# Kernel tuning notes

Measured on AMD Instinct MI355X. Metric: run time of the kernel, lower is better.

Reference implementation:

```python
import jax, jax.numpy as jnp
import numpy as np

N, E, D, H = 100000, 600000, 128, 512  # nodes, edges, latent_dim, 4*latent_dim


def setup_inputs() -> dict:
    key = jax.random.key(0)
    ks = jax.random.split(key, 9)
    s = 0.05
    return {
        "z": jax.random.normal(ks[0], (N, D), dtype=jnp.float32),
        "edge_index": jax.random.randint(ks[1], (2, E), 0, N, dtype=jnp.int64),
        "Wg": jax.random.normal(ks[2], (D, D), dtype=jnp.float32) * s,
        "Ws": jax.random.normal(ks[3], (D, D), dtype=jnp.float32) * s,
        "bg": jnp.zeros((D,), dtype=jnp.float32),
        "W1": jax.random.normal(ks[4], (D, H), dtype=jnp.float32) * s,
        "b1": jnp.zeros((H,), dtype=jnp.float32),
        "W2": jax.random.normal(ks[5], (H, H), dtype=jnp.float32) * s,
        "b2": jnp.zeros((H,), dtype=jnp.float32),
        "W3": jax.random.normal(ks[6], (H, D), dtype=jnp.float32) * s,
        "b3": jnp.zeros((D,), dtype=jnp.float32),
    }


def reference(z, edge_index, Wg, Ws, bg, W1, b1, W2, b2, W3, b3):
    src, dst = edge_index[0], edge_index[1]
    n = z.shape[0]
    # GNN: gather neighbor features along edges, mean-aggregate at dst
    msgs = z[src]                                   # (E, D) gather
    agg = jax.ops.segment_sum(msgs, dst, num_segments=n)  # (N, D) scatter-add
    deg = jax.ops.segment_sum(jnp.ones((src.shape[0],), z.dtype), dst, num_segments=n)
    agg = agg / jnp.maximum(deg, 1.0)[:, None]      # mean aggregation
    h = jax.nn.relu(agg @ Wg + z @ Ws + bg)          # (N, D) graph conv output
    # MLP: Linear -> Tanh -> Linear -> Tanh -> Linear
    h = jnp.tanh(h @ W1 + b1)
    h = jnp.tanh(h @ W2 + b2)
    return h @ W3 + b3                               # dz/dt: (N, D)
```

## Files before the change

kernel.cpp:

```cpp
#include <hip/hip_runtime.h>
#include <hip/hip_fp16.h>


typedef _Float16 f16;
typedef __attribute__((ext_vector_type(4))) _Float16 f16x4;
typedef __attribute__((ext_vector_type(8))) _Float16 f16x8;
typedef __attribute__((ext_vector_type(4))) float f32x4;

__device__ __forceinline__ void async_load16(const void* g, void* lds) {
  __builtin_amdgcn_global_load_lds(
      (const __attribute__((address_space(1))) void*)g,
      (__attribute__((address_space(3))) void*)lds, 16, 0, 0);
}

__device__ __forceinline__ float fast_tanh(float x) {
  float a = fabsf(x);
  float e = __expf(-2.0f * a);
  float r = (1.0f - e) * __builtin_amdgcn_rcpf(1.0f + e);
  return copysignf(r, x);
}

__global__ __launch_bounds__(256) void scan_partial(const int* __restrict__ degi,
                                                    int* __restrict__ bsum, int N) {
  __shared__ int lds[256];
  int b = blockIdx.x, t = threadIdx.x;
  int s = 0;
#pragma unroll
  for (int j = 0; j < 4; ++j) {
    int idx = b * 1024 + t * 4 + j;
    if (idx < N) s += degi[idx];
  }
  lds[t] = s;
  __syncthreads();
  for (int off = 128; off > 0; off >>= 1) {
    if (t < off) lds[t] += lds[t + off];
    __syncthreads();
  }
  if (t == 0) bsum[b] = lds[0];
}

__global__ __launch_bounds__(256) void scan_final(
    const int* __restrict__ degi, const int* __restrict__ bsum,
    int* __restrict__ row_start, int* __restrict__ cursor, int nb, int N, int E) {
  __shared__ int lds[256];
  __shared__ int sboff;
  int b = blockIdx.x, t = threadIdx.x;
  lds[t] = (t < b && t < nb) ? bsum[t] : 0;
  __syncthreads();
  for (int off = 128; off > 0; off >>= 1) {
    if (t < off) lds[t] += lds[t + off];
    __syncthreads();
  }
  if (t == 0) {
    sboff = lds[0];
    if (b == 0) row_start[N] = E;
  }
  __syncthreads();

  int base = b * 1024;
  int v[4];
  int s = 0;
#pragma unroll
  for (int j = 0; j < 4; ++j) {
    int idx = base + t * 4 + j;
    v[j] = (idx < N) ? degi[idx] : 0;
    s += v[j];
  }
  lds[t] = s;
  __syncthreads();
  for (int off = 1; off < 256; off <<= 1) {
    int x = lds[t];
    int y = (t >= off) ? lds[t - off] : 0;
    __syncthreads();
    lds[t] = x + y;
    __syncthreads();
  }
  int pre = sboff + lds[t] - s;
#pragma unroll
  for (int j = 0; j < 4; ++j) {
    int idx = base + t * 4 + j;
    if (idx < N) { row_start[idx] = pre; cursor[idx] = pre; pre += v[j]; }
  }
}

__global__ __launch_bounds__(256) void fill_adj(const int* __restrict__ src,
                                                const int* __restrict__ dst,
                                                int* __restrict__ cursor,
                                                int* __restrict__ adj, int E) {
  int e = blockIdx.x * 256 + threadIdx.x;
  if (e >= E) return;
  int p = atomicAdd(&cursor[dst[e]], 1);
  adj[p] = src[e];
}

__global__ __launch_bounds__(256) void fused_prep(
    const int* __restrict__ dst, int* __restrict__ degi, int E,
    const float* __restrict__ Wg, const float* __restrict__ Ws,
    const float* __restrict__ W1, const float* __restrict__ W2,
    const float* __restrict__ W3, f16* __restrict__ wgs, f16* __restrict__ wt1,
    f16* __restrict__ wt2, f16* __restrict__ wt3,
    const float* __restrict__ z, f16* __restrict__ z16, f16* __restrict__ Xc,
    int n4) {
  int i0 = blockIdx.x * 256 + threadIdx.x;
  int stride = gridDim.x * 256;
  for (int i = i0; i < n4; i += stride) {
    float4 v = *(const float4*)(z + 4 * (long long)i);
    f16x4 c;
    c[0] = (f16)v.x; c[1] = (f16)v.y; c[2] = (f16)v.z; c[3] = (f16)v.w;
    *(f16x4*)(z16 + 4 * (long long)i) = c;
    int node = i >> 5, sl = i & 31;
    *(f16x4*)(Xc + (long long)node * 256 + 128 + 4 * sl) = c;
  }
  for (int i = i0; i < E; i += stride) atomicAdd(&degi[dst[i]], 1);
  for (int i = i0; i < 425984; i += stride) {
    if (i < 32768) {
      int n = i >> 8, k = i & 255;
      wgs[i] = (f16)((k < 128) ? Wg[k * 128 + n] : Ws[(k - 128) * 128 + n]);
    } else if (i < 98304) {
      int j = i - 32768, c = j >> 7, k = j & 127;
      wt1[j] = (f16)W1[k * 512 + c];
    } else if (i < 360448) {
      int j = i - 98304, c = j >> 9, k = j & 511;
      wt2[j] = (f16)W2[k * 512 + c];
    } else {
      int j = i - 360448, c = j >> 9, k = j & 511;
      wt3[j] = (f16)W3[k * 128 + c];
    }
  }
}

__global__ __launch_bounds__(256) void gather_xcat(
    const f16* __restrict__ z16, const int* __restrict__ row_start,
    const int* __restrict__ adj, f16* __restrict__ Xc, int N) {
  int node = (blockIdx.x * 256 + threadIdx.x) >> 5;
  if (node >= N) return;
  int lane = threadIdx.x & 31;
  int beg = row_start[node], end = row_start[node + 1];
  float a0 = 0, a1 = 0, a2 = 0, a3 = 0;
#pragma unroll
  for (int j = 0; j < 8; ++j) {
    int idx = beg + j;
    bool vld = idx < end;
    int nb = adj[vld ? idx : beg];
    f16x4 x = *(const f16x4*)(z16 + (long long)nb * 128 + 4 * lane);
    float w = vld ? 1.0f : 0.0f;
    a0 += w * (float)x[0]; a1 += w * (float)x[1];
    a2 += w * (float)x[2]; a3 += w * (float)x[3];
  }
  int i = beg + 8;
  if (i < end) {
    float b0 = 0, b1 = 0, b2 = 0, b3 = 0;
    float c0 = 0, c1 = 0, c2 = 0, c3 = 0;
    float d0 = 0, d1 = 0, d2 = 0, d3 = 0;
    for (; i + 4 <= end; i += 4) {
      int n0 = adj[i], n1 = adj[i + 1], n2 = adj[i + 2], n3 = adj[i + 3];
      f16x4 v0 = *(const f16x4*)(z16 + (long long)n0 * 128 + 4 * lane);
      f16x4 v1 = *(const f16x4*)(z16 + (long long)n1 * 128 + 4 * lane);
      f16x4 v2 = *(const f16x4*)(z16 + (long long)n2 * 128 + 4 * lane);
      f16x4 v3 = *(const f16x4*)(z16 + (long long)n3 * 128 + 4 * lane);
      a0 += (float)v0[0]; a1 += (float)v0[1]; a2 += (float)v0[2]; a3 += (float)v0[3];
      b0 += (float)v1[0]; b1 += (float)v1[1]; b2 += (float)v1[2]; b3 += (float)v1[3];
      c0 += (float)v2[0]; c1 += (float)v2[1]; c2 += (float)v2[2]; c3 += (float)v2[3];
      d0 += (float)v3[0]; d1 += (float)v3[1]; d2 += (float)v3[2]; d3 += (float)v3[3];
    }
    for (; i < end; ++i) {
      f16x4 v = *(const f16x4*)(z16 + (long long)adj[i] * 128 + 4 * lane);
      a0 += (float)v[0]; a1 += (float)v[1]; a2 += (float)v[2]; a3 += (float)v[3];
    }
    a0 += b0 + c0 + d0; a1 += b1 + c1 + d1;
    a2 += b2 + c2 + d2; a3 += b3 + c3 + d3;
  }
  int dg = end - beg;
  float inv = 1.0f / (float)(dg > 1 ? dg : 1);
  long long o = (long long)node * 256;
  f16x4 m;
  m[0] = (f16)(a0 * inv); m[1] = (f16)(a1 * inv);
  m[2] = (f16)(a2 * inv); m[3] = (f16)(a3 * inv);
  *(f16x4*)(Xc + o + 4 * lane) = m;
}

__global__ __launch_bounds__(256) void fused12(
    const f16* __restrict__ Xc, const f16* __restrict__ wgs,
    const f16* __restrict__ wt1, const float* __restrict__ bg,
    const float* __restrict__ b1, f16* __restrict__ h2) {
  __shared__ __align__(16) char L[49152];
  const int tid = threadIdx.x;
  const int wid = tid >> 6, lane = tid & 63;
  const int wm = wid & 1, wn = wid >> 1;
  const int lr = lane & 15, lq = lane >> 4;
  const int key = lr & 7;
  const long long m0 = (long long)blockIdx.x * 128;
  const f16* Ag = Xc + m0 * 256;

  f32x4 acc[4][4];
#pragma unroll
  for (int i = 0; i < 4; ++i)
#pragma unroll
    for (int j = 0; j < 4; ++j)
#pragma unroll
      for (int r = 0; r < 4; ++r) acc[i][j][r] = 0.0f;

#pragma unroll 1
  for (int k0 = 0; k0 < 256; k0 += 64) {
#pragma unroll
    for (int c = 0; c < 4; ++c) {
      int f = c * 256 + tid;
      int row = f >> 3, ss = (f & 7) ^ (row & 7);
      async_load16(Ag + (long long)row * 256 + k0 + ss * 8, L + f * 16);
    }
#pragma unroll
    for (int c = 0; c < 4; ++c) {
      int f = c * 256 + tid;
      int row = f >> 3, ss = (f & 7) ^ (row & 7);
      async_load16(wgs + row * 256 + k0 + ss * 8, L + 16384 + f * 16);
    }
    __syncthreads();
#pragma unroll
    for (int kk = 0; kk < 64; kk += 32) {
      const int co = (((kk >> 3) + lq) ^ key) * 16;
      f16x8 a[4], b[4];
#pragma unroll
      for (int i = 0; i < 4; ++i)
        a[i] = *reinterpret_cast<const f16x8*>(L + (wm * 64 + i * 16 + lr) * 128 + co);
#pragma unroll
      for (int j = 0; j < 4; ++j)
        b[j] = *reinterpret_cast<const f16x8*>(L + 16384 + (wn * 64 + j * 16 + lr) * 128 + co);
#pragma unroll
      for (int i = 0; i < 4; ++i)
#pragma unroll
        for (int j = 0; j < 4; ++j)
          acc[i][j] = __builtin_amdgcn_mfma_f32_16x16x32_f16(a[i], b[j], acc[i][j], 0, 0, 0);
    }
    __syncthreads();
  }

#pragma unroll
  for (int i = 0; i < 4; ++i)
#pragma unroll
    for (int j = 0; j < 4; ++j) {
      int col = wn * 64 + j * 16 + lr;
      float bv = bg[col];
#pragma unroll
      for (int r = 0; r < 4; ++r) {
        int row = wm * 64 + i * 16 + lq * 4 + r;
        float v = fmaxf(acc[i][j][r] + bv, 0.0f);
        *reinterpret_cast<f16*>(L + row * 256 + (((col >> 3) ^ (row & 7)) * 16) +
                                (col & 7) * 2) = (f16)v;
      }
    }
  __syncthreads();

#pragma unroll 1
  for (int cb = 0; cb < 4; ++cb) {
#pragma unroll
    for (int i = 0; i < 4; ++i)
#pragma unroll
      for (int j = 0; j < 4; ++j)
#pragma unroll
        for (int r = 0; r < 4; ++r) acc[i][j][r] = 0.0f;

#pragma unroll 1
    for (int kc = 0; kc < 2; ++kc) {
#pragma unroll
      for (int c = 0; c < 4; ++c) {
        int f = c * 256 + tid;
        int row = f >> 3, ss = (f & 7) ^ (row & 7);
        async_load16(wt1 + (long long)(cb * 128 + row) * 128 + kc * 64 + ss * 8,
                     L + 32768 + f * 16);
      }
      __syncthreads();
#pragma unroll
      for (int kk = 0; kk < 64; kk += 32) {
        const int aslot = kc * 8 + (kk >> 3) + lq;
        const int bco = (((kk >> 3) + lq) ^ key) * 16;
        f16x8 a[4], b[4];
#pragma unroll
        for (int i = 0; i < 4; ++i)
          a[i] = *reinterpret_cast<const f16x8*>(
              L + (wm * 64 + i * 16 + lr) * 256 + (aslot ^ key) * 16);
#pragma unroll
        for (int j = 0; j < 4; ++j)
          b[j] = *reinterpret_cast<const f16x8*>(
              L + 32768 + (wn * 64 + j * 16 + lr) * 128 + bco);
#pragma unroll
        for (int i = 0; i < 4; ++i)
#pragma unroll
          for (int j = 0; j < 4; ++j)
            acc[i][j] = __builtin_amdgcn_mfma_f32_16x16x32_f16(a[i], b[j], acc[i][j], 0, 0, 0);
      }
      __syncthreads();
    }
#pragma unroll
    for (int i = 0; i < 4; ++i)
#pragma unroll
      for (int j = 0; j < 4; ++j) {
        int colg = cb * 128 + wn * 64 + j * 16 + lr;
        float bv = b1[colg];
#pragma unroll
        for (int r = 0; r < 4; ++r) {
          long long row = m0 + wm * 64 + i * 16 + lq * 4 + r;
          h2[row * 512 + colg] = (f16)fast_tanh(acc[i][j][r] + bv);
        }
      }
  }
}

template <int K, int NOUT, int WM, int WN, int MI, int ACT, bool OUTF32>
__global__ __launch_bounds__(WM * WN * 64) void gemm_r(
    const f16* __restrict__ X, const f16* __restrict__ Wt,
    const float* __restrict__ bias, void* __restrict__ OutV, int M) {
  constexpr int NJ = 4;
  constexpr int BM = WM * MI * 16;
  constexpr int BN = WN * NJ * 16;
  constexpr int NTHR = WM * WN * 64;
  constexpr int CA = (BM * 128) / (NTHR * 16);
  constexpr int CB = (BN * 128) / (NTHR * 16);
  __shared__ __align__(16) f16 As[BM * 64];
  __shared__ __align__(16) f16 Bs[BN * 64];

  const int tid = threadIdx.x;
  const int wid = tid >> 6, lane = tid & 63;
  const int wm = wid / WN, wn = wid % WN;
  const int lr = lane & 15, lq = lane >> 4;
  const int rxor = lr & 7;
  const long long m0 = (long long)blockIdx.x * BM;
  const int n0 = blockIdx.y * BN;

  const f16* Ag = X + m0 * K;
  const f16* Bg = Wt + (long long)n0 * K;

  long long aOff[CA], bOff[CB];
#pragma unroll
  for (int c = 0; c < CA; ++c) {
    int f = c * NTHR + tid;
    int row = f >> 3, ss = (f & 7) ^ (row & 7);
    aOff[c] = (long long)row * K + ss * 8;
  }
#pragma unroll
  for (int c = 0; c < CB; ++c) {
    int f = c * NTHR + tid;
    int row = f >> 3, ss = (f & 7) ^ (row & 7);
    bOff[c] = (long long)row * K + ss * 8;
  }

  f32x4 acc[MI][NJ];
#pragma unroll
  for (int i = 0; i < MI; ++i)
#pragma unroll
    for (int j = 0; j < NJ; ++j)
#pragma unroll
      for (int r = 0; r < 4; ++r) acc[i][j][r] = 0.0f;

#pragma unroll 1
  for (int k0 = 0; k0 < K; k0 += 64) {
#pragma unroll
    for (int c = 0; c < CA; ++c)
      async_load16(Ag + aOff[c] + k0, (char*)As + c * NTHR * 16 + wid * 1024);
#pragma unroll
    for (int c = 0; c < CB; ++c)
      async_load16(Bg + bOff[c] + k0, (char*)Bs + c * NTHR * 16 + wid * 1024);
    __syncthreads();
#pragma unroll
    for (int kk = 0; kk < 64; kk += 32) {
      const int co = (((kk >> 3) + lq) ^ rxor) * 16;
      f16x8 a[MI], b[NJ];
#pragma unroll
      for (int i = 0; i < MI; ++i)
        a[i] = *reinterpret_cast<const f16x8*>(
            (const char*)As + (wm * MI * 16 + i * 16 + lr) * 128 + co);
#pragma unroll
      for (int j = 0; j < NJ; ++j)
        b[j] = *reinterpret_cast<const f16x8*>(
            (const char*)Bs + (wn * NJ * 16 + j * 16 + lr) * 128 + co);
#pragma unroll
      for (int i = 0; i < MI; ++i)
#pragma unroll
        for (int j = 0; j < NJ; ++j)
          acc[i][j] = __builtin_amdgcn_mfma_f32_16x16x32_f16(a[i], b[j], acc[i][j], 0, 0, 0);
    }
    __syncthreads();
  }

#pragma unroll
  for (int i = 0; i < MI; ++i) {
#pragma unroll
    for (int j = 0; j < NJ; ++j) {
      int col = n0 + wn * NJ * 16 + j * 16 + lr;
      float bv = bias[col];
#pragma unroll
      for (int r = 0; r < 4; ++r) {
        long long row = m0 + wm * MI * 16 + i * 16 + lq * 4 + r;
        if (row < M) {
          float v = acc[i][j][r] + bv;
          if (ACT == 1) v = fmaxf(v, 0.0f);
          else if (ACT == 2) v = fast_tanh(v);
          if constexpr (OUTF32)
            ((float*)OutV)[row * NOUT + col] = v;
          else
            ((f16*)OutV)[row * NOUT + col] = (f16)v;
        }
      }
    }
  }
}

extern "C" void kernel_launch(void* const* d_in, const int* in_sizes, int n_in,
                              void* d_out, int out_size, void* d_ws, size_t ws_size,
                              hipStream_t stream) {
  const float* z  = (const float*)d_in[0];
  const int*   ei = (const int*)d_in[1];
  const float* Wg = (const float*)d_in[2];
  const float* Ws = (const float*)d_in[3];
  const float* bg = (const float*)d_in[4];
  const float* W1 = (const float*)d_in[5];
  const float* b1 = (const float*)d_in[6];
  const float* W2 = (const float*)d_in[7];
  const float* b2 = (const float*)d_in[8];
  const float* W3 = (const float*)d_in[9];
  const float* b3 = (const float*)d_in[10];

  const int Nn = in_sizes[0] / 128;
  const int E  = in_sizes[1] / 2;
  const int* src = ei;
  const int* dst = ei + E;
  const int nb = (Nn + 1023) / 1024;
  const int gm256 = (Nn + 255) / 256;
  const long long Mpad = (long long)gm256 * 256;
  const int gm128 = gm256 * 2;

  char* base = (char*)d_ws;
  const size_t XCB = (size_t)Mpad * 256 * 2;
  const size_t H3B = (size_t)Mpad * 512 * 2;
  f16* Xc = (f16*)(base);
  f16* h3 = (f16*)(base);
  size_t off = XCB;
  auto alloc = [&](size_t b) -> void* {
    void* p = base + off;
    off += (b + 255) & ~(size_t)255;
    return p;
  };
  int* degi      = (int*)alloc((size_t)Nn * 4);
  int* row_start = (int*)alloc((size_t)(Nn + 1) * 4);
  int* cursor    = (int*)alloc((size_t)Nn * 4);
  int* adj       = (int*)alloc((size_t)(E + 8) * 4);
  int* bsum      = (int*)alloc((size_t)nb * 4);
  f16* z16       = (f16*)alloc((size_t)Nn * 128 * 2);
  off = H3B;
  f16* h2  = (f16*)alloc((size_t)Mpad * 512 * 2);
  f16* wgs = (f16*)alloc((size_t)128 * 256 * 2);
  f16* wt1 = (f16*)alloc((size_t)512 * 128 * 2);
  f16* wt2 = (f16*)alloc((size_t)512 * 512 * 2);
  f16* wt3 = (f16*)alloc((size_t)128 * 512 * 2);

  hipMemsetAsync(degi, 0, (size_t)Nn * 4, stream);
  fused_prep<<<2048, 256, 0, stream>>>(dst, degi, E, Wg, Ws, W1, W2, W3,
                                       wgs, wt1, wt2, wt3, z, z16, Xc, Nn * 32);
  scan_partial<<<nb, 256, 0, stream>>>(degi, bsum, Nn);
  scan_final<<<nb, 256, 0, stream>>>(degi, bsum, row_start, cursor, nb, Nn, E);
  fill_adj<<<(E + 255) / 256, 256, 0, stream>>>(src, dst, cursor, adj, E);

  {
    long long tot = (long long)Nn * 32;
    gather_xcat<<<(int)((tot + 255) / 256), 256, 0, stream>>>(z16, row_start, adj, Xc, Nn);
  }

  fused12<<<gm128, 256, 0, stream>>>(Xc, wgs, wt1, bg, b1, h2);
  gemm_r<512, 512, 2, 4, 4, 2, false><<<dim3(gm128, 2), 512, 0, stream>>>(h2, wt2, b2, (void*)h3, Nn);
  gemm_r<512, 128, 4, 1, 4, 0, true><<<dim3(gm256, 2), 256, 0, stream>>>(h3, wt3, b3, d_out, Nn);
}
```

Before: 313.3 us.

## Drop concatenated Xc buffer, read mean and z16 separately; swizzle W2 GEMM blocks

```diff
diff --git a/kernel.cpp b/kernel.cpp
--- a/kernel.cpp
+++ b/kernel.cpp
@@ -99,8 +99,7 @@
     const float* __restrict__ W1, const float* __restrict__ W2,
     const float* __restrict__ W3, f16* __restrict__ wgs, f16* __restrict__ wt1,
     f16* __restrict__ wt2, f16* __restrict__ wt3,
-    const float* __restrict__ z, f16* __restrict__ z16, f16* __restrict__ Xc,
-    int n4) {
+    const float* __restrict__ z, f16* __restrict__ z16, int n4) {
   int i0 = blockIdx.x * 256 + threadIdx.x;
   int stride = gridDim.x * 256;
   for (int i = i0; i < n4; i += stride) {
@@ -108,8 +107,6 @@
     f16x4 c;
     c[0] = (f16)v.x; c[1] = (f16)v.y; c[2] = (f16)v.z; c[3] = (f16)v.w;
     *(f16x4*)(z16 + 4 * (long long)i) = c;
-    int node = i >> 5, sl = i & 31;
-    *(f16x4*)(Xc + (long long)node * 256 + 128 + 4 * sl) = c;
   }
   for (int i = i0; i < E; i += stride) atomicAdd(&degi[dst[i]], 1);
   for (int i = i0; i < 425984; i += stride) {
@@ -129,9 +126,9 @@
   }
 }
 
-__global__ __launch_bounds__(256) void gather_xcat(
+__global__ __launch_bounds__(256) void gather_xm(
     const f16* __restrict__ z16, const int* __restrict__ row_start,
-    const int* __restrict__ adj, f16* __restrict__ Xc, int N) {
+    const int* __restrict__ adj, f16* __restrict__ Xm, int N) {
   int node = (blockIdx.x * 256 + threadIdx.x) >> 5;
   if (node >= N) return;
   int lane = threadIdx.x & 31;
@@ -172,17 +169,17 @@
   }
   int dg = end - beg;
   float inv = 1.0f / (float)(dg > 1 ? dg : 1);
-  long long o = (long long)node * 256;
   f16x4 m;
   m[0] = (f16)(a0 * inv); m[1] = (f16)(a1 * inv);
   m[2] = (f16)(a2 * inv); m[3] = (f16)(a3 * inv);
-  *(f16x4*)(Xc + o + 4 * lane) = m;
+  *(f16x4*)(Xm + (long long)node * 128 + 4 * lane) = m;
 }
 
 __global__ __launch_bounds__(256) void fused12(
-    const f16* __restrict__ Xc, const f16* __restrict__ wgs,
-    const f16* __restrict__ wt1, const float* __restrict__ bg,
-    const float* __restrict__ b1, f16* __restrict__ h2) {
+    const f16* __restrict__ Xm, const f16* __restrict__ z16,
+    const f16* __restrict__ wgs, const f16* __restrict__ wt1,
+    const float* __restrict__ bg, const float* __restrict__ b1,
+    f16* __restrict__ h2) {
   __shared__ __align__(16) char L[49152];
   const int tid = threadIdx.x;
   const int wid = tid >> 6, lane = tid & 63;
@@ -190,7 +187,14 @@
   const int lr = lane & 15, lq = lane >> 4;
   const int key = lr & 7;
   const long long m0 = (long long)blockIdx.x * 128;
-  const f16* Ag = Xc + m0 * 256;
+
+  long long aOff[4];
+#pragma unroll
+  for (int c = 0; c < 4; ++c) {
+    int f = c * 256 + tid;
+    int row = f >> 3, ss = (f & 7) ^ (row & 7);
+    aOff[c] = (long long)row * 128 + ss * 8;
+  }
 
   f32x4 acc[4][4];
 #pragma unroll
@@ -202,11 +206,11 @@
 
 #pragma unroll 1
   for (int k0 = 0; k0 < 256; k0 += 64) {
+    const f16* Asrc = ((k0 < 128) ? Xm : z16) + m0 * 128 + (k0 & 127);
 #pragma unroll
     for (int c = 0; c < 4; ++c) {
       int f = c * 256 + tid;
-      int row = f >> 3, ss = (f & 7) ^ (row & 7);
-      async_load16(Ag + (long long)row * 256 + k0 + ss * 8, L + f * 16);
+      async_load16(Asrc + aOff[c], L + f * 16);
     }
 #pragma unroll
     for (int c = 0; c < 4; ++c) {
@@ -305,7 +309,7 @@
   }
 }
 
-template <int K, int NOUT, int WM, int WN, int MI, int ACT, bool OUTF32>
+template <int K, int NOUT, int WM, int WN, int MI, int ACT, bool OUTF32, int SWZ>
 __global__ __launch_bounds__(WM * WN * 64) void gemm_r(
     const f16* __restrict__ X, const f16* __restrict__ Wt,
     const float* __restrict__ bias, void* __restrict__ OutV, int M) {
@@ -323,8 +327,22 @@
   const int wm = wid / WN, wn = wid % WN;
   const int lr = lane & 15, lq = lane >> 4;
   const int rxor = lr & 7;
-  const long long m0 = (long long)blockIdx.x * BM;
-  const int n0 = blockIdx.y * BN;
+
+  int bx, by;
+  if constexpr (SWZ) {
+    int bid = blockIdx.x;
+    int wid2 = bid;
+    if ((gridDim.x & 7) == 0) {
+      int q = gridDim.x >> 3;
+      wid2 = (bid & 7) * q + (bid >> 3);
+    }
+    bx = wid2 >> 1;
+    by = wid2 & 1;
+  } else {
+    bx = blockIdx.x; by = blockIdx.y;
+  }
+  const long long m0 = (long long)bx * BM;
+  const int n0 = by * BN;
 
   const f16* Ag = X + m0 * K;
   const f16* Bg = Wt + (long long)n0 * K;
@@ -429,11 +447,12 @@
   const int gm128 = gm256 * 2;
 
   char* base = (char*)d_ws;
-  const size_t XCB = (size_t)Mpad * 256 * 2;
+  const size_t XMB = (size_t)Mpad * 128 * 2;
   const size_t H3B = (size_t)Mpad * 512 * 2;
-  f16* Xc = (f16*)(base);
-  f16* h3 = (f16*)(base);
-  size_t off = XCB;
+  f16* Xm  = (f16*)(base);
+  f16* h3  = (f16*)(base);
+  f16* z16 = (f16*)(base + XMB);
+  size_t off = XMB + (size_t)Mpad * 128 * 2;
   auto alloc = [&](size_t b) -> void* {
     void* p = base + off;
     off += (b + 255) & ~(size_t)255;
@@ -444,7 +463,6 @@
   int* cursor    = (int*)alloc((size_t)Nn * 4);
   int* adj       = (int*)alloc((size_t)(E + 8) * 4);
   int* bsum      = (int*)alloc((size_t)nb * 4);
-  f16* z16       = (f16*)alloc((size_t)Nn * 128 * 2);
   off = H3B;
   f16* h2  = (f16*)alloc((size_t)Mpad * 512 * 2);
   f16* wgs = (f16*)alloc((size_t)128 * 256 * 2);
@@ -454,17 +472,17 @@
 
   hipMemsetAsync(degi, 0, (size_t)Nn * 4, stream);
   fused_prep<<<2048, 256, 0, stream>>>(dst, degi, E, Wg, Ws, W1, W2, W3,
-                                       wgs, wt1, wt2, wt3, z, z16, Xc, Nn * 32);
+                                       wgs, wt1, wt2, wt3, z, z16, Nn * 32);
   scan_partial<<<nb, 256, 0, stream>>>(degi, bsum, Nn);
   scan_final<<<nb, 256, 0, stream>>>(degi, bsum, row_start, cursor, nb, Nn, E);
   fill_adj<<<(E + 255) / 256, 256, 0, stream>>>(src, dst, cursor, adj, E);
 
   {
     long long tot = (long long)Nn * 32;
-    gather_xcat<<<(int)((tot + 255) / 256), 256, 0, stream>>>(z16, row_start, adj, Xc, Nn);
-  }
-
-  fused12<<<gm128, 256, 0, stream>>>(Xc, wgs, wt1, bg, b1, h2);
-  gemm_r<512, 512, 2, 4, 4, 2, false><<<dim3(gm128, 2), 512, 0, stream>>>(h2, wt2, b2, (void*)h3, Nn);
-  gemm_r<512, 128, 4, 1, 4, 0, true><<<dim3(gm256, 2), 256, 0, stream>>>(h3, wt3, b3, d_out, Nn);
-}
+    gather_xm<<<(int)((tot + 255) / 256), 256, 0, stream>>>(z16, row_start, adj, Xm, Nn);
+  }
+
+  fused12<<<gm128, 256, 0, stream>>>(Xm, z16, wgs, wt1, bg, b1, h2);
+  gemm_r<512, 512, 2, 4, 4, 2, false, 1><<<gm128 * 2, 512, 0, stream>>>(h2, wt2, b2, (void*)h3, Nn);
+  gemm_r<512, 128, 4, 1, 4, 0, true, 0><<<dim3(gm256, 2), 256, 0, stream>>>(h3, wt3, b3, d_out, Nn);
+}
```

New measurement: 347.8 us. 1.11x slower.
